# Performance work log

Measured on AMD Instinct MI355X. Metric: run time of the kernel, lower is better.

The kernel has to match this reference:

```python
import jax, jax.numpy as jnp
import numpy as np

B, T, HID = 8, 2048, 1024
NH, MD = 16, 16
UFC = 2  # len(use_for_context) = ['lr', 'rl']
MAT_EPS = 1e-5
VEC_EPS = 1e-6
SQRT_MD = float(np.sqrt(MD))


def setup_inputs() -> dict:
    key = jax.random.key(0)
    ks = jax.random.split(key, 5)
    s_in = 1.0 / np.sqrt(HID)
    s_out = 1.0 / np.sqrt(NH * MD * UFC)
    return {
        "hidden_states": jax.random.normal(ks[0], (B, T, HID), jnp.float32),
        "W_mat": jax.random.uniform(ks[1], (HID, NH * MD * MD), jnp.float32, -s_in, s_in),
        "b_mat": jax.random.uniform(ks[2], (NH * MD * MD,), jnp.float32, -s_in, s_in),
        "W_out": jax.random.uniform(ks[3], (NH * MD * UFC, HID), jnp.float32, -s_out, s_out),
        "b_out": jax.random.uniform(ks[4], (HID,), jnp.float32, -s_out, s_out),
    }


def _scan_vectors(m, v0, reverse):
    """Sequential matrix-vector recurrence with per-step L2 normalization.
    m: (T, B*NH, d, d); v0: (B*NH, d). Returns history (T, B*NH, d)
    (equal to torch history[1:] for lr, and reversed(history[1:]) for rl)."""
    def step(v, m_t):
        nv = jnp.einsum('bij,bj->bi', m_t, v)
        nv = nv / (jnp.linalg.norm(nv, axis=-1, keepdims=True) + VEC_EPS)
        return nv, nv
    _, hist = jax.lax.scan(step, v0, m, reverse=reverse)
    return hist


def reference(hidden_states, W_mat, b_mat, W_out, b_out):
    # predict_matrix: fc_to_mat + Frobenius matrix normalization ([-2,-1] branch)
    m = hidden_states @ W_mat + b_mat                       # (B, T, NH*MD*MD)
    m = m.reshape(B, T, NH, MD, MD).transpose(1, 0, 2, 3, 4)  # (T, B, NH, d, d)
    fro = jnp.linalg.norm(m, axis=(-2, -1), keepdims=True)
    m_norm = m / (fro + MAT_EPS) * SQRT_MD
    m_norm = m_norm.reshape(T, B * NH, MD, MD)

    # init_type == 'one': v[..., 0, :] = 1 -> e_0
    v0 = jnp.zeros((B * NH, MD), jnp.float32).at[:, 0].set(1.0)

    v_lr = _scan_vectors(m_norm, v0, reverse=False)  # (T, B*NH, d)
    v_rl = _scan_vectors(m_norm, v0, reverse=True)   # (T, B*NH, d)

    def to_bthd(v):
        return v.reshape(T, B, NH, MD).transpose(1, 0, 2, 3)  # (B, T, NH, d)

    x = jnp.concatenate([to_bthd(v_lr), to_bthd(v_rl)], axis=-1)  # (B, T, NH, 2d)
    # networks_for_heads == 'common': flatten heads, Linear, gelu (exact erf form)
    x = x.reshape(B, T, NH * MD * UFC) @ W_out + b_out
    return jax.nn.gelu(x, approximate=False)
```

## Files before the change

### kernel.cpp

```cpp
#include <hip/hip_runtime.h>
#include <math.h>

#define Tdim 2048
#define HIDd 1024
#define NHd 16
#define NCOL 4096
#define Cn 64
#define Ln 32
#define LSTR 40
#define KCAT 3072
#define KB 6144

typedef _Float16 f16x4  __attribute__((ext_vector_type(4)));
typedef _Float16 f16x8  __attribute__((ext_vector_type(8)));
typedef float    f32x4  __attribute__((ext_vector_type(4)));

typedef __attribute__((address_space(1))) void gvoid_t;
typedef __attribute__((address_space(3))) void lvoid_t;

__global__ __launch_bounds__(256) void conv_A_kernel(const float* __restrict__ hs,
                                                     _Float16* __restrict__ Ac)
{
    const size_t i = ((size_t)blockIdx.x * 256 + threadIdx.x) * 8;
    const size_t r = i >> 10, k = i & 1023;
    const float4 x0 = *(const float4*)(hs + i);
    const float4 x1 = *(const float4*)(hs + i + 4);
    const float v[8] = {x0.x, x0.y, x0.z, x0.w, x1.x, x1.y, x1.z, x1.w};
    f16x8 h, hm, l;
#pragma unroll
    for (int j = 0; j < 8; ++j) {
        const _Float16 hh = (_Float16)v[j];
        h[j]  = hh;
        hm[j] = (_Float16)(v[j] * 0.03125f);
        l[j]  = (_Float16)((v[j] - (float)hh) * 32.0f);
    }
    _Float16* o = Ac + r * KCAT + k;
    *(f16x8*)(o)        = h;
    *(f16x8*)(o + 1024) = hm;
    *(f16x8*)(o + 2048) = l;
}

__global__ __launch_bounds__(256) void conv_B_kernel(const float* __restrict__ W,
                                                     _Float16* __restrict__ Bc)
{
    __shared__ float t[32][33];
    const int tx = threadIdx.x & 31, ty = threadIdx.x >> 5;
    const int n0 = blockIdx.x * 32, k0 = blockIdx.y * 32;
#pragma unroll
    for (int i = 0; i < 4; ++i)
        t[ty + i * 8][tx] = W[(size_t)(k0 + ty + i * 8) * NCOL + n0 + tx];
    __syncthreads();
#pragma unroll
    for (int i = 0; i < 4; ++i) {
        const float w = t[tx][ty + i * 8];
        const _Float16 h = (_Float16)w;
        const size_t o = (size_t)(n0 + ty + i * 8) * KCAT + k0 + tx;
        Bc[o]        = h;
        Bc[o + 1024] = (_Float16)((w - (float)h) * 32.0f);
        Bc[o + 2048] = (_Float16)((float)h * 0.03125f);
    }
}

__global__ __launch_bounds__(256) void conv_W2T_kernel(const float* __restrict__ W,
                                                       _Float16* __restrict__ WT)
{
    __shared__ float t[32][33];
    const int tx = threadIdx.x & 31, ty = threadIdx.x >> 5;
    const int n0 = blockIdx.x * 32, k0 = blockIdx.y * 32;
#pragma unroll
    for (int i = 0; i < 4; ++i)
        t[ty + i * 8][tx] = W[(size_t)(k0 + ty + i * 8) * 1024 + n0 + tx];
    __syncthreads();
#pragma unroll
    for (int i = 0; i < 4; ++i)
        WT[(size_t)(n0 + ty + i * 8) * 512 + k0 + tx] = (_Float16)t[tx][ty + i * 8];
}

#define MFMA_PHASE(CPH) \
    _Pragma("unroll") \
    for (int m2_ = 0; m2_ < 2; ++m2_) { \
        _Pragma("unroll") \
        for (int nt_ = 0; nt_ < 4; ++nt_) { \
            acc[(CPH)*2 + m2_][nt_] = __builtin_amdgcn_mfma_f32_16x16x32_f16(af[m2_][0], bf[nt_][0], acc[(CPH)*2 + m2_][nt_], 0, 0, 0); \
            acc[(CPH)*2 + m2_][nt_] = __builtin_amdgcn_mfma_f32_16x16x32_f16(af[m2_][1], bf[nt_][1], acc[(CPH)*2 + m2_][nt_], 0, 0, 0); \
        } \
    }

#define PHASE(BUF, CPH, STAGE_EXPR, DOGATE) do { \
    af[0][0] = readA(BUF, (CPH)*2,     0); \
    af[0][1] = readA(BUF, (CPH)*2,     1); \
    af[1][0] = readA(BUF, (CPH)*2 + 1, 0); \
    af[1][1] = readA(BUF, (CPH)*2 + 1, 1); \
    if ((CPH) == 0) { \
        _Pragma("unroll") \
        for (int nt_ = 0; nt_ < 4; ++nt_) { bf[nt_][0] = readB(BUF, nt_, 0); bf[nt_][1] = readB(BUF, nt_, 1); } \
    } \
    STAGE_EXPR; \
    asm volatile("s_barrier" ::: "memory"); \
    asm volatile("s_waitcnt lgkmcnt(0)" ::: "memory"); \
    __builtin_amdgcn_sched_barrier(0); \
    __builtin_amdgcn_s_setprio(1); \
    MFMA_PHASE(CPH) \
    __builtin_amdgcn_s_setprio(0); \
    if (DOGATE) { \
        if (notlast) asm volatile("s_waitcnt vmcnt(6)" ::: "memory"); \
        else         asm volatile("s_waitcnt vmcnt(0)" ::: "memory"); \
    } \
    asm volatile("s_barrier" ::: "memory"); \
} while (0)

__global__ __launch_bounds__(512, 2) void gemm1_8ph(const _Float16* __restrict__ A,
                                                    const _Float16* __restrict__ B,
                                                    const float* __restrict__ bias,
                                                    float* __restrict__ Mout)
{
    __shared__ __align__(16) _Float16 sA[2][256 * 64];
    __shared__ __align__(16) _Float16 sB[2][256 * 64];
    const int tid = threadIdx.x;
    const int lane = tid & 63;
    const int wid = tid >> 6;
    const int wm = wid >> 2, wn = wid & 3;
    const int q = lane >> 4, ln = lane & 15;
    const int col0 = blockIdx.x * 256;
    const int row0 = blockIdx.y * 256;

    const char* Ab = (const char*)A + (size_t)row0 * KB;
    const char* Bb = (const char*)B + (size_t)col0 * KB;

    auto stage_chunk = [&](const char* g, int fr, int kt, char* ldsbase) {
        const int rr = tid >> 3;
        const int cb = (tid & 7) << 4;
        const char* src = g + (size_t)(fr + rr) * KB + (size_t)kt * 128 + (cb ^ ((rr & 7) << 4));
        char* dst = ldsbase + ((tid >> 6) << 10);
        __builtin_amdgcn_global_load_lds((gvoid_t*)src, (lvoid_t*)dst, 16, 0, 0);
    };
    auto stageA2g = [&](int b, int t, int h) {
        stage_chunk(Ab, h * 64,       t, (char*)&sA[b][0] + (size_t)(h * 64) * 128);
        stage_chunk(Ab, 128 + h * 64, t, (char*)&sA[b][0] + (size_t)(128 + h * 64) * 128);
    };
    auto stageB2 = [&](int b, int t, int h) {
        stage_chunk(Bb, h * 128,      t, (char*)&sB[b][0] + (size_t)(h * 128) * 128);
        stage_chunk(Bb, h * 128 + 64, t, (char*)&sB[b][0] + (size_t)(h * 128 + 64) * 128);
    };
    auto readA = [&](int b, int mf, int ks) -> f16x8 {
        const int r = wm * 128 + mf * 16 + ln;
        return *(const f16x8*)((const char*)&sA[b][0] + r * 128 + ((ks * 64 + q * 16) ^ ((r & 7) << 4)));
    };
    auto readB = [&](int b, int nt, int ks) -> f16x8 {
        const int r = wn * 64 + nt * 16 + ln;
        return *(const f16x8*)((const char*)&sB[b][0] + r * 128 + ((ks * 64 + q * 16) ^ ((r & 7) << 4)));
    };

    stageB2(0, 0, 0); stageB2(0, 0, 1); stageA2g(0, 0, 0); stageA2g(0, 0, 1);
    stageB2(1, 1, 0); stageB2(1, 1, 1); stageA2g(1, 1, 0);

    f32x4 acc[8][4];
    const f32x4 z4 = {0.f, 0.f, 0.f, 0.f};
#pragma unroll
    for (int mf = 0; mf < 8; ++mf)
#pragma unroll
        for (int nt = 0; nt < 4; ++nt) acc[mf][nt] = z4;

    asm volatile("s_waitcnt vmcnt(6)" ::: "memory");
    asm volatile("s_barrier" ::: "memory");

    f16x8 af[2][2];
    f16x8 bf[4][2];

#pragma unroll 1
    for (int it = 0; it < 24; ++it) {
        const int t0 = it * 2;
        const bool notlast = (it != 23);
        PHASE(0, 0, (stageA2g(1, t0 + 1, 1)), 0);
        PHASE(0, 1, (notlast ? stageB2(0, t0 + 2, 0) : (void)0), 0);
        PHASE(0, 2, (notlast ? stageB2(0, t0 + 2, 1) : (void)0), 0);
        PHASE(0, 3, (notlast ? stageA2g(0, t0 + 2, 0) : (void)0), 1);
        PHASE(1, 0, (notlast ? stageA2g(0, t0 + 2, 1) : (void)0), 0);
        PHASE(1, 1, (notlast ? stageB2(1, t0 + 3, 0) : (void)0), 0);
        PHASE(1, 2, (notlast ? stageB2(1, t0 + 3, 1) : (void)0), 0);
        PHASE(1, 3, (notlast ? stageA2g(1, t0 + 3, 0) : (void)0), 1);
    }

#pragma unroll
    for (int nt = 0; nt < 4; ++nt) {
        const int c = col0 + wn * 64 + nt * 16 + ln;
        const float bv = bias[c];
        const int h = c >> 8, e = c & 255;
#pragma unroll
        for (int mf = 0; mf < 8; ++mf) {
#pragma unroll
            for (int r = 0; r < 4; ++r) {
                const int row = row0 + wm * 128 + mf * 16 + q * 4 + r;
                const int bbl = row >> 11, t = row & 2047;
                Mout[((size_t)(bbl * 16 + h) * Tdim + t) * 256 + e] = acc[mf][nt][r] + bv;
            }
        }
    }
}

__global__ __launch_bounds__(128) void stageA2_mfma(float* __restrict__ m,
                                                    float* __restrict__ q, int SS)
{
    __shared__ float Ml[Ln * 256];
    const int tid = threadIdx.x;
    const int dir = tid >> 6;
    const int lane = tid & 63;
    const int qd = lane >> 4, ln = lane & 15;
    const int sc = blockIdx.x;
    const int seq = sc >> 6, c = sc & (Cn - 1);
    float* mp = m + ((size_t)seq * Tdim + c * Ln) * 256;

    {
        const float4* src = (const float4*)mp;
        float4* dst = (float4*)Ml;
#pragma unroll
        for (int i = 0; i < 16; ++i)
            dst[tid + i * 128] = src[tid + i * 128];
    }
    __syncthreads();

    float v[4];
#pragma unroll
    for (int r = 0; r < 4; ++r) v[r] = (qd * 4 + r == ln) ? 1.0f : 0.0f;

    const int s0 = dir ? (Ln - 1) : 0;
    const int ds = dir ? -1 : 1;

    int t = s0;
    float4 arow = *(const float4*)&Ml[t * 256 + ln * 16 + qd * 4];
    float f2 = arow.x*arow.x + arow.y*arow.y + arow.z*arow.z + arow.w*arow.w;
#pragma unroll
    for (int off = 1; off < 64; off <<= 1) f2 += __shfl_xor(f2, off);
    float sm = 4.0f * rsqrtf(f2 + 1e-12f);

    for (int s = 0; s < Ln; ++s) {
        const int tcur = t;
        f16x4 mh, mlo;
        const float ar[4] = {arow.x * sm, arow.y * sm, arow.z * sm, arow.w * sm};
#pragma unroll
        for (int i = 0; i < 4; ++i) {
            const _Float16 h = (_Float16)ar[i];
            mh[i] = h; mlo[i] = (_Float16)((ar[i] - (float)h) * 1024.0f);
        }
        float smn = sm;
        if (s + 1 < Ln) {
            t += ds;
            arow = *(const float4*)&Ml[t * 256 + ln * 16 + qd * 4];
            float f2n = arow.x*arow.x + arow.y*arow.y + arow.z*arow.z + arow.w*arow.w;
#pragma unroll
            for (int off = 1; off < 64; off <<= 1) f2n += __shfl_xor(f2n, off);
            smn = 4.0f * rsqrtf(f2n + 1e-12f);
        }
        f16x4 qh, ql;
#pragma unroll
        for (int r = 0; r < 4; ++r) {
            const _Float16 h = (_Float16)v[r];
            qh[r] = h; ql[r] = (_Float16)((v[r] - (float)h) * 1024.0f);
        }
        f32x4 a1 = {0.f,0.f,0.f,0.f}, a2 = {0.f,0.f,0.f,0.f};
        a1 = __builtin_amdgcn_mfma_f32_16x16x16f16(mh,  qh, a1, 0, 0, 0);
        a2 = __builtin_amdgcn_mfma_f32_16x16x16f16(mh,  ql, a2, 0, 0, 0);
        a2 = __builtin_amdgcn_mfma_f32_16x16x16f16(mlo, qh, a2, 0, 0, 0);
#pragma unroll
        for (int r = 0; r < 4; ++r) v[r] = a1[r] + a2[r] * (1.0f / 1024.0f);

        if (s & 1) {
            float mx = 0.f;
#pragma unroll
            for (int r = 0; r < 4; ++r) mx = fmaxf(mx, fabsf(v[r]));
#pragma unroll
            for (int off = 1; off < 64; off <<= 1) mx = fmaxf(mx, __shfl_xor(mx, off));
            const float inv = 1.0f / (mx + 1e-30f);
#pragma unroll
            for (int r = 0; r < 4; ++r) v[r] *= inv;
        }
        _Float16* Pp = (_Float16*)((char*)mp + (size_t)tcur * 1024 + dir * 512);
#pragma unroll
        for (int r = 0; r < 4; ++r)
            Pp[(qd * 4 + r) * 16 + ln] = (_Float16)v[r];
        sm = smn;
    }

    float ss = 0.f;
#pragma unroll
    for (int r = 0; r < 4; ++r) ss += v[r] * v[r];
#pragma unroll
    for (int off = 1; off < 64; off <<= 1) ss += __shfl_xor(ss, off);
    const float sl = 1.0f / (sqrtf(ss) + 1e-30f);
    float* qo = q + ((size_t)(dir * SS + seq) * Cn + c) * 256;
#pragma unroll
    for (int r = 0; r < 4; ++r)
        qo[(qd * 4 + r) * 16 + ln] = v[r] * sl;
}

__global__ __launch_bounds__(64) void stageB_kernel(const float* __restrict__ q,
                                                    float* __restrict__ vs, int SS)
{
    const int lane = threadIdx.x & 63;
    const int i = lane & 15;
    const int chain = blockIdx.x;
    const int dir = (chain >= SS) ? 1 : 0;
    const int seq = chain - dir * SS;
    const float* qb = q + (size_t)(dir * SS + seq) * Cn * 256;
    float* vb = vs + (size_t)(dir * SS + seq) * Cn * 16;

    float myw = (i == 0) ? 1.0f : 0.0f;
    float wv[16];
#pragma unroll
    for (int k2 = 0; k2 < 16; ++k2) wv[k2] = (k2 == 0) ? 1.0f : 0.0f;

    int cc = dir ? (Cn - 1) : 0;
    const float* Qp = qb + (size_t)cc * 256 + i * 16;
    float4 q0 = *(const float4*)(Qp + 0);
    float4 q1 = *(const float4*)(Qp + 4);
    float4 q2 = *(const float4*)(Qp + 8);
    float4 q3 = *(const float4*)(Qp + 12);

    for (int s = 0; s < Cn; ++s) {
        vb[cc * 16 + i] = myw;
        float nv = q0.x*wv[0] + q0.y*wv[1] + q0.z*wv[2] + q0.w*wv[3]
                 + q1.x*wv[4] + q1.y*wv[5] + q1.z*wv[6] + q1.w*wv[7]
                 + q2.x*wv[8] + q2.y*wv[9] + q2.z*wv[10] + q2.w*wv[11]
                 + q3.x*wv[12] + q3.y*wv[13] + q3.z*wv[14] + q3.w*wv[15];
        if (s + 1 < Cn) {
            const int ccn = dir ? (Cn - 2 - s) : (s + 1);
            const float* Qn = qb + (size_t)ccn * 256 + i * 16;
            q0 = *(const float4*)(Qn + 0);
            q1 = *(const float4*)(Qn + 4);
            q2 = *(const float4*)(Qn + 8);
            q3 = *(const float4*)(Qn + 12);
        }
        float s2 = nv * nv;
        s2 += __shfl_xor(s2, 1); s2 += __shfl_xor(s2, 2);
        s2 += __shfl_xor(s2, 4); s2 += __shfl_xor(s2, 8);
        const float wn = nv / (sqrtf(s2) + 1e-20f);
        myw = wn;
#pragma unroll
        for (int k2 = 0; k2 < 16; ++k2) wv[k2] = __shfl(wn, (lane & 48) | k2);
        cc = dir ? (Cn - 2 - s) : (s + 1);
    }
}

__global__ __launch_bounds__(256) void stageC2_kernel(const float* __restrict__ m,
                                                      const float* __restrict__ vs,
                                                      _Float16* __restrict__ x, int SS)
{
    const int tid = threadIdx.x;
    const int wave = tid >> 6, lane = tid & 63;
    const int dsc = blockIdx.x * 4 + wave;
    const int dirseq = dsc >> 6, c = dsc & (Cn - 1);
    const int dir = (dirseq >= SS) ? 1 : 0;
    const int seq = dirseq - dir * SS;
    const int bbl = seq >> 4, h = seq & 15;
    const _Float16* Pp = (const _Float16*)((const char*)m
                       + ((size_t)seq * Tdim + c * Ln) * 1024 + dir * 512);
    const float* vp = vs + (size_t)dsc * 16;

    float v[16];
#pragma unroll
    for (int k = 0; k < 16; ++k) v[k] = vp[k];

    const int tt = lane >> 4, j = lane & 15;
    const int t0 = c * Ln;
#pragma unroll
    for (int g = 0; g < 8; ++g) {
        const int s = g * 4 + tt;
        const _Float16* pr = Pp + (size_t)s * 512 + j * 16;
        const f16x8 p0 = *(const f16x8*)(pr);
        const f16x8 p1 = *(const f16x8*)(pr + 8);
        float nv = 0.f;
#pragma unroll
        for (int k = 0; k < 8; ++k) nv += (float)p0[k] * v[k];
#pragma unroll
        for (int k = 0; k < 8; ++k) nv += (float)p1[k] * v[k + 8];
        float s2 = nv * nv;
        s2 += __shfl_xor(s2, 1); s2 += __shfl_xor(s2, 2);
        s2 += __shfl_xor(s2, 4); s2 += __shfl_xor(s2, 8);
        const float vn = nv / (sqrtf(s2) + 1e-6f);
        const int t = t0 + s;
        x[(((size_t)bbl * Tdim + t) * NHd + h) * 32 + dir * 16 + j] = (_Float16)vn;
    }
}

__global__ __launch_bounds__(256) void gemm2_f16(const _Float16* __restrict__ A,
                                                 const _Float16* __restrict__ BT,
                                                 const float* __restrict__ bias,
                                                 float* __restrict__ out, int row0)
{
    __shared__ _Float16 Al[128 * LSTR];
    __shared__ _Float16 Bl[128 * LSTR];
    const int tid = threadIdx.x;
    const int wave = tid >> 6, lane = tid & 63;
    const int wm = wave & 1, wn = wave >> 1;
    const int qd = lane >> 4, ln = lane & 15;
    const int r0 = blockIdx.y * 128;
    const int c0 = blockIdx.x * 128;

    f32x4 acc[4][4] = {{{0.f,0.f,0.f,0.f}}};

    const int sr = tid >> 2, sc = tid & 3;
    const _Float16* Ag = A  + (size_t)(r0 + sr) * 512 + sc * 8;
    const _Float16* Bg = BT + (size_t)(c0 + sr) * 512 + sc * 8;
    _Float16* Alw = &Al[sr * LSTR + sc * 8];
    _Float16* Blw = &Bl[sr * LSTR + sc * 8];

    for (int k0 = 0; k0 < 512; k0 += 32) {
        const f16x8 a0 = *(const f16x8*)(Ag + k0);
        const f16x8 a1 = *(const f16x8*)(Ag + (size_t)64 * 512 + k0);
        const f16x8 b0 = *(const f16x8*)(Bg + k0);
        const f16x8 b1 = *(const f16x8*)(Bg + (size_t)64 * 512 + k0);
        __syncthreads();
        *(f16x8*)(Alw)             = a0;
        *(f16x8*)(Alw + 64 * LSTR) = a1;
        *(f16x8*)(Blw)             = b0;
        *(f16x8*)(Blw + 64 * LSTR) = b1;
        __syncthreads();
        f16x8 af[4], bfr[4];
#pragma unroll
        for (int mt = 0; mt < 4; ++mt)
            af[mt] = *(const f16x8*)&Al[(wm * 64 + mt * 16 + ln) * LSTR + qd * 8];
#pragma unroll
        for (int nt = 0; nt < 4; ++nt)
            bfr[nt] = *(const f16x8*)&Bl[(wn * 64 + nt * 16 + ln) * LSTR + qd * 8];
#pragma unroll
        for (int mt = 0; mt < 4; ++mt)
#pragma unroll
            for (int nt = 0; nt < 4; ++nt)
                acc[mt][nt] = __builtin_amdgcn_mfma_f32_16x16x32_f16(af[mt], bfr[nt], acc[mt][nt], 0, 0, 0);
    }
#pragma unroll
    for (int nt = 0; nt < 4; ++nt) {
        const int c = c0 + wn * 64 + nt * 16 + ln;
        const float bv = bias[c];
#pragma unroll
        for (int mt = 0; mt < 4; ++mt) {
#pragma unroll
            for (int r = 0; r < 4; ++r) {
                const int row = r0 + wm * 64 + mt * 16 + qd * 4 + r;
                float v = acc[mt][nt][r] + bv;
                v = 0.5f * v * (1.0f + erff(v * 0.70710678118654752f));
                out[(size_t)(row0 + row) * 1024 + c] = v;
            }
        }
    }
}

extern "C" void kernel_launch(void* const* d_in, const int* in_sizes, int n_in,
                              void* d_out, int out_size, void* d_ws, size_t ws_size,
                              hipStream_t stream)
{
    const float* hs    = (const float*)d_in[0];
    const float* W_mat = (const float*)d_in[1];
    const float* b_mat = (const float*)d_in[2];
    const float* W_out = (const float*)d_in[3];
    const float* b_out = (const float*)d_in[4];
    float* out = (float*)d_out;

    const size_t per_bb = (32ull << 20) + (2ull << 20) + (12ull << 20) + (128ull << 10);
    const size_t wbase  = 25ull << 20;
    int nbb = 8;
    while (nbb > 1 && ws_size < wbase + (size_t)nbb * per_bb) nbb >>= 1;

    char* base = (char*)d_ws;
    _Float16* W2T = (_Float16*)base;
    _Float16* Bc  = (_Float16*)(base + (1ull << 20));
    size_t off = wbase;
    float* m  = (float*)(base + off);  off += (size_t)nbb * (32ull << 20);
    float* qx = (float*)(base + off);  off += (size_t)nbb * (2ull << 20);
    _Float16* Ac = (_Float16*)(base + off); off += (size_t)nbb * (12ull << 20);
    float* vs = (float*)(base + off);

    conv_B_kernel<<<dim3(128, 32), 256, 0, stream>>>(W_mat, Bc);
    conv_W2T_kernel<<<dim3(32, 16), 256, 0, stream>>>(W_out, W2T);

    for (int bb0 = 0; bb0 < 8; bb0 += nbb) {
        const int row0 = bb0 * Tdim;
        const int SS = nbb * 16;
        conv_A_kernel<<<nbb * 1024, 256, 0, stream>>>(hs + (size_t)row0 * HIDd, Ac);
        gemm1_8ph<<<dim3(16, nbb * 8), 512, 0, stream>>>(Ac, Bc, b_mat, m);
        stageA2_mfma<<<SS * Cn, 128, 0, stream>>>(m, qx, SS);
        stageB_kernel<<<2 * SS, 64, 0, stream>>>(qx, vs, SS);
        stageC2_kernel<<<SS * Cn / 2, 256, 0, stream>>>(m, vs, (_Float16*)qx, SS);
        gemm2_f16<<<dim3(8, nbb * 16), 256, 0, stream>>>((_Float16*)qx, W2T, b_out, out, row0);
    }
}
```

Measured before the change: 877.9 us.

## Fuse chunk-local scan stage into GEMM1 epilogue via shared memory

The GEMM1 epilogue now stages each 128-row half of the output tile in LDS. Eight waves then run the per-chunk forward and backward matrix-vector scans directly on that data, writing the fp16 partial histories and chunk summary vectors. This removes the fp32 write of the full matrix tensor and its re-read by a separate stageA2 kernel, plus one launch. In exchange the GEMM blocks carry a serial 32-step epilogue twice, which lengthens them and may hurt occupancy or overlap with the next tiles.

```diff
diff --git a/kernel.cpp b/kernel.cpp
--- a/kernel.cpp
+++ b/kernel.cpp
@@ -112,10 +112,10 @@
 __global__ __launch_bounds__(512, 2) void gemm1_8ph(const _Float16* __restrict__ A,
                                                     const _Float16* __restrict__ B,
                                                     const float* __restrict__ bias,
-                                                    float* __restrict__ Mout)
-{
-    __shared__ __align__(16) _Float16 sA[2][256 * 64];
-    __shared__ __align__(16) _Float16 sB[2][256 * 64];
+                                                    float* __restrict__ Mout,
+                                                    float* __restrict__ qout, int SS)
+{
+    __shared__ __align__(16) _Float16 sAB[4][256 * 64];
     const int tid = threadIdx.x;
     const int lane = tid & 63;
     const int wid = tid >> 6;
@@ -135,20 +135,20 @@
         __builtin_amdgcn_global_load_lds((gvoid_t*)src, (lvoid_t*)dst, 16, 0, 0);
     };
     auto stageA2g = [&](int b, int t, int h) {
-        stage_chunk(Ab, h * 64,       t, (char*)&sA[b][0] + (size_t)(h * 64) * 128);
-        stage_chunk(Ab, 128 + h * 64, t, (char*)&sA[b][0] + (size_t)(128 + h * 64) * 128);
+        stage_chunk(Ab, h * 64,       t, (char*)&sAB[b][0] + (size_t)(h * 64) * 128);
+        stage_chunk(Ab, 128 + h * 64, t, (char*)&sAB[b][0] + (size_t)(128 + h * 64) * 128);
     };
     auto stageB2 = [&](int b, int t, int h) {
-        stage_chunk(Bb, h * 128,      t, (char*)&sB[b][0] + (size_t)(h * 128) * 128);
-        stage_chunk(Bb, h * 128 + 64, t, (char*)&sB[b][0] + (size_t)(h * 128 + 64) * 128);
+        stage_chunk(Bb, h * 128,      t, (char*)&sAB[2 + b][0] + (size_t)(h * 128) * 128);
+        stage_chunk(Bb, h * 128 + 64, t, (char*)&sAB[2 + b][0] + (size_t)(h * 128 + 64) * 128);
     };
     auto readA = [&](int b, int mf, int ks) -> f16x8 {
         const int r = wm * 128 + mf * 16 + ln;
-        return *(const f16x8*)((const char*)&sA[b][0] + r * 128 + ((ks * 64 + q * 16) ^ ((r & 7) << 4)));
+        return *(const f16x8*)((const char*)&sAB[b][0] + r * 128 + ((ks * 64 + q * 16) ^ ((r & 7) << 4)));
     };
     auto readB = [&](int b, int nt, int ks) -> f16x8 {
         const int r = wn * 64 + nt * 16 + ln;
-        return *(const f16x8*)((const char*)&sB[b][0] + r * 128 + ((ks * 64 + q * 16) ^ ((r & 7) << 4)));
+        return *(const f16x8*)((const char*)&sAB[2 + b][0] + r * 128 + ((ks * 64 + q * 16) ^ ((r & 7) << 4)));
     };
 
     stageB2(0, 0, 0); stageB2(0, 0, 1); stageA2g(0, 0, 0); stageA2g(0, 0, 1);
@@ -181,116 +181,104 @@
         PHASE(1, 3, (notlast ? stageA2g(1, t0 + 3, 0) : (void)0), 1);
     }
 
-#pragma unroll
-    for (int nt = 0; nt < 4; ++nt) {
-        const int c = col0 + wn * 64 + nt * 16 + ln;
-        const float bv = bias[c];
-        const int h = c >> 8, e = c & 255;
-#pragma unroll
-        for (int mf = 0; mf < 8; ++mf) {
+    float* Mf = (float*)&sAB[0][0];
+    const int seq = ((row0 >> 11) << 4) + blockIdx.x;
+    const int cc   = wid & 3;
+    const int dirw = wid >> 2;
+    float bv[4];
+#pragma unroll
+    for (int nt = 0; nt < 4; ++nt) bv[nt] = bias[col0 + wn * 64 + nt * 16 + ln];
+
+#pragma unroll 1
+    for (int half = 0; half < 2; ++half) {
+        __syncthreads();
+        if (wm == half) {
+#pragma unroll
+            for (int mf = 0; mf < 8; ++mf)
+#pragma unroll
+                for (int nt = 0; nt < 4; ++nt)
+#pragma unroll
+                    for (int r = 0; r < 4; ++r)
+                        Mf[(mf * 16 + q * 4 + r) * 256 + wn * 64 + nt * 16 + ln]
+                            = acc[mf][nt][r] + bv[nt];
+        }
+        __syncthreads();
+
+        const int cblk = half * 4 + cc;
+        const int tb   = cblk * 32 - half * 128;
+        float v[4];
+#pragma unroll
+        for (int r = 0; r < 4; ++r) v[r] = (q * 4 + r == ln) ? 1.0f : 0.0f;
+
+        int tl = dirw ? (tb + 31) : tb;
+        const int ds = dirw ? -1 : 1;
+        float4 arow = *(const float4*)&Mf[tl * 256 + ln * 16 + q * 4];
+        float f2 = arow.x*arow.x + arow.y*arow.y + arow.z*arow.z + arow.w*arow.w;
+#pragma unroll
+        for (int off = 1; off < 64; off <<= 1) f2 += __shfl_xor(f2, off);
+        float sm = 4.0f * rsqrtf(f2 + 1e-12f);
+
+        for (int s = 0; s < Ln; ++s) {
+            const int tabs = (row0 & 2047) + (dirw ? (cblk * 32 + 31 - s) : (cblk * 32 + s));
+            f16x4 mh, mlo;
+            const float ar[4] = {arow.x * sm, arow.y * sm, arow.z * sm, arow.w * sm};
+#pragma unroll
+            for (int i = 0; i < 4; ++i) {
+                const _Float16 h = (_Float16)ar[i];
+                mh[i] = h; mlo[i] = (_Float16)((ar[i] - (float)h) * 1024.0f);
+            }
+            float smn = sm;
+            if (s + 1 < Ln) {
+                tl += ds;
+                arow = *(const float4*)&Mf[tl * 256 + ln * 16 + q * 4];
+                float f2n = arow.x*arow.x + arow.y*arow.y + arow.z*arow.z + arow.w*arow.w;
+#pragma unroll
+                for (int off = 1; off < 64; off <<= 1) f2n += __shfl_xor(f2n, off);
+                smn = 4.0f * rsqrtf(f2n + 1e-12f);
+            }
+            f16x4 qh, ql;
 #pragma unroll
             for (int r = 0; r < 4; ++r) {
-                const int row = row0 + wm * 128 + mf * 16 + q * 4 + r;
-                const int bbl = row >> 11, t = row & 2047;
-                Mout[((size_t)(bbl * 16 + h) * Tdim + t) * 256 + e] = acc[mf][nt][r] + bv;
+                const _Float16 h = (_Float16)v[r];
+                qh[r] = h; ql[r] = (_Float16)((v[r] - (float)h) * 1024.0f);
             }
+            f32x4 a1 = {0.f,0.f,0.f,0.f}, a2 = {0.f,0.f,0.f,0.f};
+            a1 = __builtin_amdgcn_mfma_f32_16x16x16f16(mh,  qh, a1, 0, 0, 0);
+            a2 = __builtin_amdgcn_mfma_f32_16x16x16f16(mh,  ql, a2, 0, 0, 0);
+            a2 = __builtin_amdgcn_mfma_f32_16x16x16f16(mlo, qh, a2, 0, 0, 0);
+#pragma unroll
+            for (int r = 0; r < 4; ++r) v[r] = a1[r] + a2[r] * (1.0f / 1024.0f);
+
+            if (s & 1) {
+                float mx = 0.f;
+#pragma unroll
+                for (int r = 0; r < 4; ++r) mx = fmaxf(mx, fabsf(v[r]));
+#pragma unroll
+                for (int off = 1; off < 64; off <<= 1) mx = fmaxf(mx, __shfl_xor(mx, off));
+                const float inv = 1.0f / (mx + 1e-30f);
+#pragma unroll
+                for (int r = 0; r < 4; ++r) v[r] *= inv;
+            }
+            _Float16* Pp = (_Float16*)((char*)Mout
+                         + ((size_t)seq * Tdim + tabs) * 1024 + dirw * 512);
+#pragma unroll
+            for (int r = 0; r < 4; ++r)
+                Pp[(q * 4 + r) * 16 + ln] = (_Float16)v[r];
+            sm = smn;
         }
-    }
-}
-
-__global__ __launch_bounds__(128) void stageA2_mfma(float* __restrict__ m,
-                                                    float* __restrict__ q, int SS)
-{
-    __shared__ float Ml[Ln * 256];
-    const int tid = threadIdx.x;
-    const int dir = tid >> 6;
-    const int lane = tid & 63;
-    const int qd = lane >> 4, ln = lane & 15;
-    const int sc = blockIdx.x;
-    const int seq = sc >> 6, c = sc & (Cn - 1);
-    float* mp = m + ((size_t)seq * Tdim + c * Ln) * 256;
-
-    {
-        const float4* src = (const float4*)mp;
-        float4* dst = (float4*)Ml;
-#pragma unroll
-        for (int i = 0; i < 16; ++i)
-            dst[tid + i * 128] = src[tid + i * 128];
-    }
-    __syncthreads();
-
-    float v[4];
-#pragma unroll
-    for (int r = 0; r < 4; ++r) v[r] = (qd * 4 + r == ln) ? 1.0f : 0.0f;
-
-    const int s0 = dir ? (Ln - 1) : 0;
-    const int ds = dir ? -1 : 1;
-
-    int t = s0;
-    float4 arow = *(const float4*)&Ml[t * 256 + ln * 16 + qd * 4];
-    float f2 = arow.x*arow.x + arow.y*arow.y + arow.z*arow.z + arow.w*arow.w;
-#pragma unroll
-    for (int off = 1; off < 64; off <<= 1) f2 += __shfl_xor(f2, off);
-    float sm = 4.0f * rsqrtf(f2 + 1e-12f);
-
-    for (int s = 0; s < Ln; ++s) {
-        const int tcur = t;
-        f16x4 mh, mlo;
-        const float ar[4] = {arow.x * sm, arow.y * sm, arow.z * sm, arow.w * sm};
-#pragma unroll
-        for (int i = 0; i < 4; ++i) {
-            const _Float16 h = (_Float16)ar[i];
-            mh[i] = h; mlo[i] = (_Float16)((ar[i] - (float)h) * 1024.0f);
-        }
-        float smn = sm;
-        if (s + 1 < Ln) {
-            t += ds;
-            arow = *(const float4*)&Ml[t * 256 + ln * 16 + qd * 4];
-            float f2n = arow.x*arow.x + arow.y*arow.y + arow.z*arow.z + arow.w*arow.w;
-#pragma unroll
-            for (int off = 1; off < 64; off <<= 1) f2n += __shfl_xor(f2n, off);
-            smn = 4.0f * rsqrtf(f2n + 1e-12f);
-        }
-        f16x4 qh, ql;
-#pragma unroll
-        for (int r = 0; r < 4; ++r) {
-            const _Float16 h = (_Float16)v[r];
-            qh[r] = h; ql[r] = (_Float16)((v[r] - (float)h) * 1024.0f);
-        }
-        f32x4 a1 = {0.f,0.f,0.f,0.f}, a2 = {0.f,0.f,0.f,0.f};
-        a1 = __builtin_amdgcn_mfma_f32_16x16x16f16(mh,  qh, a1, 0, 0, 0);
-        a2 = __builtin_amdgcn_mfma_f32_16x16x16f16(mh,  ql, a2, 0, 0, 0);
-        a2 = __builtin_amdgcn_mfma_f32_16x16x16f16(mlo, qh, a2, 0, 0, 0);
-#pragma unroll
-        for (int r = 0; r < 4; ++r) v[r] = a1[r] + a2[r] * (1.0f / 1024.0f);
-
-        if (s & 1) {
-            float mx = 0.f;
-#pragma unroll
-            for (int r = 0; r < 4; ++r) mx = fmaxf(mx, fabsf(v[r]));
-#pragma unroll
-            for (int off = 1; off < 64; off <<= 1) mx = fmaxf(mx, __shfl_xor(mx, off));
-            const float inv = 1.0f / (mx + 1e-30f);
-#pragma unroll
-            for (int r = 0; r < 4; ++r) v[r] *= inv;
-        }
-        _Float16* Pp = (_Float16*)((char*)mp + (size_t)tcur * 1024 + dir * 512);
+
+        float ss = 0.f;
+#pragma unroll
+        for (int r = 0; r < 4; ++r) ss += v[r] * v[r];
+#pragma unroll
+        for (int off = 1; off < 64; off <<= 1) ss += __shfl_xor(ss, off);
+        const float sl = 1.0f / (sqrtf(ss) + 1e-30f);
+        const int cabs = ((row0 & 2047) >> 5) + cblk;
+        float* qo = qout + ((size_t)(dirw * SS + seq) * Cn + cabs) * 256;
 #pragma unroll
         for (int r = 0; r < 4; ++r)
-            Pp[(qd * 4 + r) * 16 + ln] = (_Float16)v[r];
-        sm = smn;
-    }
-
-    float ss = 0.f;
-#pragma unroll
-    for (int r = 0; r < 4; ++r) ss += v[r] * v[r];
-#pragma unroll
-    for (int off = 1; off < 64; off <<= 1) ss += __shfl_xor(ss, off);
-    const float sl = 1.0f / (sqrtf(ss) + 1e-30f);
-    float* qo = q + ((size_t)(dir * SS + seq) * Cn + c) * 256;
-#pragma unroll
-    for (int r = 0; r < 4; ++r)
-        qo[(qd * 4 + r) * 16 + ln] = v[r] * sl;
+            qo[(q * 4 + r) * 16 + ln] = v[r] * sl;
+    }
 }
 
 __global__ __launch_bounds__(64) void stageB_kernel(const float* __restrict__ q,
@@ -477,8 +465,7 @@
         const int row0 = bb0 * Tdim;
         const int SS = nbb * 16;
         conv_A_kernel<<<nbb * 1024, 256, 0, stream>>>(hs + (size_t)row0 * HIDd, Ac);
-        gemm1_8ph<<<dim3(16, nbb * 8), 512, 0, stream>>>(Ac, Bc, b_mat, m);
-        stageA2_mfma<<<SS * Cn, 128, 0, stream>>>(m, qx, SS);
+        gemm1_8ph<<<dim3(16, nbb * 8), 512, 0, stream>>>(Ac, Bc, b_mat, m, qx, SS);
         stageB_kernel<<<2 * SS, 64, 0, stream>>>(qx, vs, SS);
         stageC2_kernel<<<SS * Cn / 2, 256, 0, stream>>>(m, vs, (_Float16*)qx, SS);
         gemm2_f16<<<dim3(8, nbb * 16), 256, 0, stream>>>((_Float16*)qx, W2T, b_out, out, row0);
```

Measured after the change: 786.3 us. 1.12x faster.
